# Kernel tuning notes

Hardware: AMD Instinct MI355X
Metric: run time of the kernel (lower is better)

The kernel has to match this reference:

```python
import jax, jax.numpy as jnp
import numpy as np

N, IN_DIM, ENC_DIM, K = 16384, 1024, 256, 8192


def setup_inputs() -> dict:
    key = jax.random.key(0)
    ks = jax.random.split(key, 10)
    s = 0.02
    return {
        "x": jax.random.normal(ks[0], (N, IN_DIM), dtype=jnp.float32),
        "enc_w1": jax.random.normal(ks[1], (IN_DIM, ENC_DIM), dtype=jnp.float32) * s,
        "enc_b1": jnp.zeros((ENC_DIM,), dtype=jnp.float32),
        "enc_w2": jax.random.normal(ks[2], (ENC_DIM, ENC_DIM), dtype=jnp.float32) * s,
        "enc_b2": jnp.zeros((ENC_DIM,), dtype=jnp.float32),
        "codewords": jax.random.normal(ks[3], (K, ENC_DIM), dtype=jnp.float32),
        "dec_w1": jax.random.normal(ks[4], (ENC_DIM, ENC_DIM), dtype=jnp.float32) * s,
        "dec_b1": jnp.zeros((ENC_DIM,), dtype=jnp.float32),
        "dec_w2": jax.random.normal(ks[5], (ENC_DIM, IN_DIM), dtype=jnp.float32) * s,
        "dec_b2": jnp.zeros((IN_DIM,), dtype=jnp.float32),
    }


def reference(x, enc_w1, enc_b1, enc_w2, enc_b2, codewords, dec_w1, dec_b1, dec_w2, dec_b2):
    # Encoder: Linear -> ReLU -> Linear -> ReLU
    h = jax.nn.relu(x @ enc_w1 + enc_b1)
    encoded = jax.nn.relu(h @ enc_w2 + enc_b2)  # [N, ENC_DIM]

    # VQ: full Euclidean distance matrix (torch.cdist, p=2), argmin, gather
    x2 = jnp.sum(encoded * encoded, axis=1, keepdims=True)          # [N, 1]
    c2 = jnp.sum(codewords * codewords, axis=1)                     # [K]
    d2 = x2 + c2[None, :] - 2.0 * (encoded @ codewords.T)           # [N, K]
    distances = jnp.sqrt(jnp.maximum(d2, 0.0))
    quantized_indices = jnp.argmin(distances, axis=1)               # [N] int
    quantized_distances = jnp.take_along_axis(
        distances, quantized_indices[:, None], axis=1)[:, 0]        # [N]
    quantized = codewords[quantized_indices]                        # [N, ENC_DIM]

    # Decoder: Linear -> ReLU -> Linear
    g = jax.nn.relu(quantized @ dec_w1 + dec_b1)
    reconstructed = g @ dec_w2 + dec_b2                              # [N, IN_DIM]
    return quantized_indices, quantized_distances, reconstructed, quantized
```

## Files before the change

### kernel.cpp

```cpp
#include <hip/hip_runtime.h>
#include <hip/hip_bf16.h>

#define NROWS   16384
#define IN_DIM  1024
#define ENC_DIM 256
#define KCW     8192
#define NCB     32

typedef __attribute__((ext_vector_type(8))) short short8v;
typedef __attribute__((ext_vector_type(4))) float f32x4;
typedef unsigned long long u64;
typedef unsigned int u32;

__device__ __forceinline__ unsigned short f2bf_rne(float x) {
    unsigned u = __float_as_uint(x);
    unsigned r = (u + 0x7fffu + ((u >> 16) & 1u)) >> 16;
    return (unsigned short)r;
}
__device__ __forceinline__ float bf2f(unsigned short h) {
    return __uint_as_float(((unsigned)h) << 16);
}
__device__ __forceinline__ int lex_lt(float d, int i, float D, int I) {
    return (d < D) || (d == D && i < I);
}
__device__ __forceinline__ void t2mrg(u64& b1, u64& b2, u64 c1, u64 c2) {
    u64 hi = (b1 > c1) ? b1 : c1;
    u64 lo2 = (b2 < c2) ? b2 : c2;
    b1 = (b1 < c1) ? b1 : c1;
    b2 = (hi < lo2) ? hi : lo2;
}
__device__ __forceinline__ void gload16(const void* g, void* l) {
    __builtin_amdgcn_global_load_lds(
        (__attribute__((address_space(1))) void*)g,
        (__attribute__((address_space(3))) void*)l, 16, 0, 0);
}

template<int K>
__device__ __forceinline__ void split_body(const float* __restrict__ src,
                                           unsigned short* __restrict__ dst,
                                           int e) {
    int row = e / (K / 4), kq = (e % (K / 4)) * 4;
    float4 v = ((const float4*)src)[e];
    ushort4 hi, lo;
    hi.x = f2bf_rne(v.x); lo.x = f2bf_rne(v.x - bf2f(hi.x));
    hi.y = f2bf_rne(v.y); lo.y = f2bf_rne(v.y - bf2f(hi.y));
    hi.z = f2bf_rne(v.z); lo.z = f2bf_rne(v.z - bf2f(hi.z));
    hi.w = f2bf_rne(v.w); lo.w = f2bf_rne(v.w - bf2f(hi.w));
    const int m = (row & 7) << 4;
    char* rowp = (char*)(dst + (size_t)row * (2 * K));
    int bh = kq * 2, bl = (K + kq) * 2;
    *(ushort4*)(rowp + ((bh & ~127) | ((bh & 127) ^ m))) = hi;
    *(ushort4*)(rowp + ((bl & ~127) | ((bl & 127) ^ m))) = lo;
}

template<int K>
__device__ __forceinline__ void tsplit_body(const float* __restrict__ W,
                                            unsigned short* __restrict__ Wt,
                                            int Ncols, int idx) {
    int n = idx / (K / 4), k4 = (idx % (K / 4)) * 4;
    float vx = W[(size_t)(k4 + 0) * Ncols + n];
    float vy = W[(size_t)(k4 + 1) * Ncols + n];
    float vz = W[(size_t)(k4 + 2) * Ncols + n];
    float vw = W[(size_t)(k4 + 3) * Ncols + n];
    ushort4 hi, lo;
    hi.x = f2bf_rne(vx); lo.x = f2bf_rne(vx - bf2f(hi.x));
    hi.y = f2bf_rne(vy); lo.y = f2bf_rne(vy - bf2f(hi.y));
    hi.z = f2bf_rne(vz); lo.z = f2bf_rne(vz - bf2f(hi.z));
    hi.w = f2bf_rne(vw); lo.w = f2bf_rne(vw - bf2f(hi.w));
    const int m = (n & 7) << 4;
    char* rp = (char*)(Wt + (size_t)n * (2 * K));
    int bh = k4 * 2, bl = (K + k4) * 2;
    *(ushort4*)(rp + ((bh & ~127) | ((bh & 127) ^ m))) = hi;
    *(ushort4*)(rp + ((bl & ~127) | ((bl & 127) ^ m))) = lo;
}

__device__ __forceinline__ void rownorm_body(const float* __restrict__ A,
                                             float* __restrict__ out, int idx) {
    int wid = idx >> 6, lane = idx & 63;
    float4 v = *(const float4*)(A + (size_t)wid * 256 + lane * 4);
    float s = (v.x * v.x + v.y * v.y) + (v.z * v.z + v.w * v.w);
#pragma unroll
    for (int off = 1; off < 64; off <<= 1) s += __shfl_xor(s, off);
    if (lane == 0) out[wid] = s;
}

__global__ __launch_bounds__(256)
void prep_all(const float* __restrict__ ew1, const float* __restrict__ ew2,
              const float* __restrict__ dw1, const float* __restrict__ dw2,
              const float* __restrict__ cw,
              unsigned short* __restrict__ w1ts, unsigned short* __restrict__ ew2t,
              unsigned short* __restrict__ dw1t, unsigned short* __restrict__ dw2t,
              unsigned short* __restrict__ Be,   float* __restrict__ c2) {
    int idx = blockIdx.x * 256 + threadIdx.x;
    if (idx < 65536)        { tsplit_body<1024>(ew1, w1ts, 256, idx); }
    else if (idx < 81920)   { tsplit_body<256>(ew2, ew2t, 256, idx - 65536); }
    else if (idx < 98304)   { tsplit_body<256>(dw1, dw1t, 256, idx - 81920); }
    else if (idx < 163840)  { tsplit_body<256>(dw2, dw2t, 1024, idx - 98304); }
    else if (idx < 688128)  { split_body<256>(cw, Be, idx - 163840); }
    else if (idx < 1212416) { rownorm_body(cw, c2, idx - 688128); }
}

struct MMP {
    const unsigned short* A;
    const unsigned short* Bt;
    const float* bias;
    float* C;
    unsigned short* Cs;
    int N, ars, brs, crs, KQ, EPI, gx;
};

__device__ void mm_device512(const MMP p, int bx, int by, int tid) {
    __shared__ __align__(16) unsigned short As[128][64];
    __shared__ __align__(16) unsigned short Bs[128][64];
    const int lane = tid & 63;
    const int wid = tid >> 6;
    const int wr = wid >> 2, wc = wid & 3;
    const int brow = by * 128;
    const int bcol = bx * 128;
    const int K = p.KQ * 64;

    f32x4 acc[4][2] = {};

    const int fr = tid >> 3;
    const int fk = (tid & 7) * 8;
    const int swz = (lane & 7) << 4;
    const int arow = wr * 64 + (lane & 15);
    const int brw  = wc * 32 + (lane & 15);
    const int klane = (lane >> 4) * 16;

    bool first = true;
#pragma unroll
    for (int term = 0; term < 3; ++term) {
        const int kaT = (term == 2) ? K : 0;
        const int kbT = (term == 1) ? K : 0;
        for (int kq = 0; kq < p.KQ; ++kq) {
            if (!first) __syncthreads();
            first = false;
            const int ka0 = kaT + kq * 64;
            const int kb0 = kbT + kq * 64;
#pragma unroll
            for (int l = 0; l < 2; ++l) {
                gload16(p.A  + (size_t)(brow + l * 64 + fr) * p.ars + ka0 + fk,
                        (char*)&As[0][0] + l * 8192 + tid * 16);
                gload16(p.Bt + (size_t)(bcol + l * 64 + fr) * p.brs + kb0 + fk,
                        (char*)&Bs[0][0] + l * 8192 + tid * 16);
            }
            __syncthreads();
#pragma unroll
            for (int kk = 0; kk < 2; ++kk) {
                const int kb = (kk * 64 + klane) ^ swz;
                short8v af[4], bfv[2];
#pragma unroll
                for (int mi = 0; mi < 4; mi++)
                    af[mi] = *(const short8v*)((const char*)&As[arow + mi * 16][0] + kb);
#pragma unroll
                for (int ni = 0; ni < 2; ni++)
                    bfv[ni] = *(const short8v*)((const char*)&Bs[brw + ni * 16][0] + kb);
#pragma unroll
                for (int mi = 0; mi < 4; mi++)
#pragma unroll
                    for (int ni = 0; ni < 2; ni++)
                        acc[mi][ni] = __builtin_amdgcn_mfma_f32_16x16x32_bf16(
                            af[mi], bfv[ni], acc[mi][ni], 0, 0, 0);
            }
        }
    }

#pragma unroll
    for (int mi = 0; mi < 4; mi++) {
#pragma unroll
        for (int q = 0; q < 4; q++) {
            int row = brow + wr * 64 + mi * 16 + (lane >> 4) * 4 + q;
            const int m = (row & 7) << 4;
            char* rp = (char*)(p.Cs + (size_t)row * p.crs);
#pragma unroll
            for (int ni = 0; ni < 2; ni++) {
                int col = bcol + wc * 32 + ni * 16 + (lane & 15);
                float v = acc[mi][ni][q] + p.bias[col];
                if (p.EPI != 3) v = fmaxf(v, 0.f);
                if (p.EPI & 1) p.C[(size_t)row * p.N + col] = v;
                if (p.EPI != 3) {
                    unsigned short hi = f2bf_rne(v);
                    int bh = col * 2;
                    *(unsigned short*)(rp + ((bh & ~127) | ((bh & 127) ^ m))) = hi;
                    if (p.EPI == 2) {
                        unsigned short lo = f2bf_rne(v - bf2f(hi));
                        int bl = (256 + col) * 2;
                        *(unsigned short*)(rp + ((bl & ~127) | ((bl & 127) ^ m))) = lo;
                    }
                }
            }
        }
    }
}

__global__ __launch_bounds__(512)
void mm_pair(MMP p0, MMP p1, int n0) {
    if ((int)blockIdx.x < n0) {
        mm_device512(p0, blockIdx.x % p0.gx, blockIdx.x / p0.gx, threadIdx.x);
    } else {
        int b = blockIdx.x - n0;
        mm_device512(p1, b % p1.gx, b / p1.gx, threadIdx.x);
    }
}

__global__ __launch_bounds__(512)
void enc1_fused(const float* __restrict__ x,
                const unsigned short* __restrict__ w1ts,
                const float* __restrict__ bias,
                unsigned short* __restrict__ Hs) {
    __shared__ __align__(16) unsigned short Ah[64][64];
    __shared__ __align__(16) unsigned short Al[64][64];
    __shared__ __align__(16) unsigned short Bh[256][64];
    __shared__ __align__(16) unsigned short Bl[256][64];
    const int tid = threadIdx.x;
    const int lane = tid & 63;
    const int wid = tid >> 6;
    const int wr = wid >> 2, wc = wid & 3;
    const int brow = blockIdx.x * 64;

    f32x4 acc[2][4] = {};

    const int fr = tid >> 3;
    const int fk = (tid & 7) * 8;
    const int swz = (lane & 7) << 4;
    const int arow = wr * 32 + (lane & 15);
    const int brw  = wc * 64 + (lane & 15);
    const int klane = (lane >> 4) * 16;
    const int aoff = fr * 128 + ((fk * 2) ^ ((fr & 7) << 4));

    float4 c0, c1, n0, n1;
    {
        const float* xp = x + (size_t)(brow + fr) * 1024 + fk;
        c0 = *(const float4*)xp; c1 = *(const float4*)(xp + 4);
    }

    for (int s = 0; s < 16; ++s) {
        const int k0 = s * 64;
        if (s) __syncthreads();
        {
            float vv[8] = { c0.x, c0.y, c0.z, c0.w, c1.x, c1.y, c1.z, c1.w };
            short8v uh, ul;
#pragma unroll
            for (int i = 0; i < 8; i++) {
                unsigned short h = f2bf_rne(vv[i]);
                uh[i] = (short)h;
                ul[i] = (short)f2bf_rne(vv[i] - bf2f(h));
            }
            *(short8v*)((char*)&Ah[0][0] + aoff) = uh;
            *(short8v*)((char*)&Al[0][0] + aoff) = ul;
        }
#pragma unroll
        for (int l = 0; l < 4; ++l) {
            gload16(w1ts + (size_t)(l * 64 + fr) * 2048 + k0 + fk,
                    (char*)&Bh[0][0] + l * 8192 + tid * 16);
            gload16(w1ts + (size_t)(l * 64 + fr) * 2048 + 1024 + k0 + fk,
                    (char*)&Bl[0][0] + l * 8192 + tid * 16);
        }
        if (s + 1 < 16) {
            const float* xp = x + (size_t)(brow + fr) * 1024 + k0 + 64 + fk;
            n0 = *(const float4*)xp; n1 = *(const float4*)(xp + 4);
        }
        __syncthreads();
#pragma unroll
        for (int kk = 0; kk < 2; ++kk) {
            const int kb = (kk * 64 + klane) ^ swz;
            short8v ah[2], al[2], bh[4], bl[4];
#pragma unroll
            for (int mi = 0; mi < 2; mi++) {
                ah[mi] = *(const short8v*)((const char*)&Ah[arow + mi * 16][0] + kb);
                al[mi] = *(const short8v*)((const char*)&Al[arow + mi * 16][0] + kb);
            }
#pragma unroll
            for (int ni = 0; ni < 4; ni++) {
                bh[ni] = *(const short8v*)((const char*)&Bh[brw + ni * 16][0] + kb);
                bl[ni] = *(const short8v*)((const char*)&Bl[brw + ni * 16][0] + kb);
            }
#pragma unroll
            for (int mi = 0; mi < 2; mi++)
#pragma unroll
                for (int ni = 0; ni < 4; ni++) {
                    acc[mi][ni] = __builtin_amdgcn_mfma_f32_16x16x32_bf16(
                        ah[mi], bh[ni], acc[mi][ni], 0, 0, 0);
                    acc[mi][ni] = __builtin_amdgcn_mfma_f32_16x16x32_bf16(
                        ah[mi], bl[ni], acc[mi][ni], 0, 0, 0);
                    acc[mi][ni] = __builtin_amdgcn_mfma_f32_16x16x32_bf16(
                        al[mi], bh[ni], acc[mi][ni], 0, 0, 0);
                }
        }
        c0 = n0; c1 = n1;
    }

#pragma unroll
    for (int mi = 0; mi < 2; mi++) {
#pragma unroll
        for (int q = 0; q < 4; q++) {
            int row = brow + wr * 32 + mi * 16 + (lane >> 4) * 4 + q;
            const int m = (row & 7) << 4;
            char* rp = (char*)(Hs + (size_t)row * 512);
#pragma unroll
            for (int ni = 0; ni < 4; ni++) {
                int col = wc * 64 + ni * 16 + (lane & 15);
                float v = fmaxf(acc[mi][ni][q] + bias[col], 0.f);
                unsigned short hi = f2bf_rne(v);
                unsigned short lo = f2bf_rne(v - bf2f(hi));
                int bh_ = col * 2, bl_ = (256 + col) * 2;
                *(unsigned short*)(rp + ((bh_ & ~127) | ((bh_ & 127) ^ m))) = hi;
                *(unsigned short*)(rp + ((bl_ & ~127) | ((bl_ & 127) ^ m))) = lo;
            }
        }
    }
}

__global__ __launch_bounds__(512)
void vq_mfma(const unsigned short* __restrict__ Ae,
             const unsigned short* __restrict__ Be,
             const float* __restrict__ c2,
             ulonglong2* __restrict__ part) {
    __shared__ __align__(16) unsigned short As[128][64];
    __shared__ __align__(16) unsigned short Bs[256][64];
    __shared__ u32 s1[128][4];
    __shared__ u32 s2[128][4];

    const int tid  = threadIdx.x;
    const int lane = tid & 63;
    const int wid  = tid >> 6;
    const int wr   = wid >> 2;
    const int wc   = wid & 3;
    const int brow = blockIdx.y * 128;
    const int bcol = blockIdx.x * 256;

    f32x4 acc[4][4] = {};

    const int fr = tid >> 3;
    const int fk = (tid & 7) * 8;
    const int swz   = (lane & 7) << 4;
    const int arow  = wr * 64 + (lane & 15);
    const int brw   = wc * 64 + (lane & 15);
    const int klane = (lane >> 4) * 16;

    for (int s = 0; s < 4; ++s) {
        const int k0 = s * 64;
        if (s) __syncthreads();
#pragma unroll
        for (int l = 0; l < 2; ++l)
            gload16(Ae + (size_t)(brow + l * 64 + fr) * 256 + k0 + fk,
                    (char*)&As[0][0] + l * 8192 + tid * 16);
#pragma unroll
        for (int l = 0; l < 4; ++l)
            gload16(Be + (size_t)(bcol + l * 64 + fr) * 512 + k0 + fk,
                    (char*)&Bs[0][0] + l * 8192 + tid * 16);
        __syncthreads();
#pragma unroll
        for (int kk = 0; kk < 2; ++kk) {
            const int kb = (kk * 64 + klane) ^ swz;
            short8v af[4], bfv[4];
#pragma unroll
            for (int mi = 0; mi < 4; mi++)
                af[mi] = *(const short8v*)((const char*)&As[arow + mi * 16][0] + kb);
#pragma unroll
            for (int ni = 0; ni < 4; ni++)
                bfv[ni] = *(const short8v*)((const char*)&Bs[brw + ni * 16][0] + kb);
#pragma unroll
            for (int mi = 0; mi < 4; mi++)
#pragma unroll
                for (int ni = 0; ni < 4; ni++)
                    acc[mi][ni] = __builtin_amdgcn_mfma_f32_16x16x32_bf16(
                        bfv[ni], af[mi], acc[mi][ni], 0, 0, 0);
        }
    }

    const int qrow = lane & 15;
    const int cq   = (lane >> 4) * 4;
    float4 c2q[4];
#pragma unroll
    for (int ni = 0; ni < 4; ni++)
        c2q[ni] = *(const float4*)&c2[bcol + wc * 64 + ni * 16 + cq];

#pragma unroll
    for (int mi = 0; mi < 4; mi++) {
        u32 b1 = 0xFFFFFFFFu, b2 = 0xFFFFFFFFu;
#pragma unroll
        for (int ni = 0; ni < 4; ni++) {
            const float* cp = (const float*)&c2q[ni];
#pragma unroll
            for (int r = 0; r < 4; r++) {
                float dk = fmaf(-2.0f, acc[mi][ni][r], cp[r]);
                dk = fmaxf(dk, 0.0f);
                u32 k = (__float_as_uint(dk) & ~255u)
                      | (u32)(wc * 64 + ni * 16 + cq + r);
                u32 mx = max(k, b1);
                b1 = min(k, b1);
                b2 = min(mx, b2);
            }
        }
#pragma unroll
        for (int off = 16; off < 64; off <<= 1) {
            u32 o1 = __shfl_xor(b1, off);
            u32 o2 = __shfl_xor(b2, off);
            u32 mx = max(b1, o1);
            b1 = min(b1, o1);
            b2 = min(min(b2, o2), mx);
        }
        if (lane < 16) {
            int rl = wr * 64 + mi * 16 + qrow;
            s1[rl][wc] = b1;
            s2[rl][wc] = b2;
        }
    }
    __syncthreads();
    if (tid < 128) {
        u32 b1 = s1[tid][0], b2 = s2[tid][0];
#pragma unroll
        for (int w = 1; w < 4; w++) {
            u32 c1 = s1[tid][w], cc2 = s2[tid][w];
            u32 mx = max(b1, c1);
            b1 = min(b1, c1);
            b2 = min(min(b2, cc2), mx);
        }
        ulonglong2 pk;
        pk.x = ((u64)b1 << 32) | (u32)(bcol + (b1 & 255u));
        pk.y = ((u64)b2 << 32) | (u32)(bcol + (b2 & 255u));
        part[(size_t)(brow + tid) * NCB + blockIdx.x] = pk;
    }
}

__global__ __launch_bounds__(512)
void combine_dec2(const ulonglong2* __restrict__ part,
                  const float* __restrict__ enc,
                  const float* __restrict__ cw,
                  const float* __restrict__ c2,
                  float* __restrict__ outIdx,
                  float* __restrict__ outDist,
                  int* __restrict__ idx32,
                  float* __restrict__ outQ,
                  MMP pd, int nd2) {
    if ((int)blockIdx.x < nd2) {
        mm_device512(pd, blockIdx.x % pd.gx, blockIdx.x / pd.gx, threadIdx.x);
        return;
    }
    const int row  = (blockIdx.x - nd2) * 8 + (threadIdx.x >> 6);
    const int lane = threadIdx.x & 63;

    u64 b1 = ~0ull, b2 = ~0ull;
    if (lane < NCB) {
        ulonglong2 pk = part[(size_t)row * NCB + lane];
        b1 = pk.x; b2 = pk.y;
    }
#pragma unroll
    for (int off = 1; off < 64; off <<= 1) {
        u64 c1 = __shfl_xor(b1, off);
        u64 cc2 = __shfl_xor(b2, off);
        t2mrg(b1, b2, c1, cc2);
    }
    int j1 = (int)(b1 & 0xffffffffu);
    int j2 = (int)(b2 & 0xffffffffu);

    float4 e4 = ((const float4*)(enc + (size_t)row * 256))[lane];
    float4 w1 = ((const float4*)(cw + (size_t)j1 * 256))[lane];
    float4 w2 = ((const float4*)(cw + (size_t)j2 * 256))[lane];
    float s1 = fmaf(e4.x, w1.x, fmaf(e4.y, w1.y, fmaf(e4.z, w1.z, e4.w * w1.w)));
    float s2 = fmaf(e4.x, w2.x, fmaf(e4.y, w2.y, fmaf(e4.z, w2.z, e4.w * w2.w)));
    float sx = (e4.x * e4.x + e4.y * e4.y) + (e4.z * e4.z + e4.w * e4.w);
#pragma unroll
    for (int off = 1; off < 64; off <<= 1) {
        s1 += __shfl_xor(s1, off);
        s2 += __shfl_xor(s2, off);
        sx += __shfl_xor(sx, off);
    }
    float d1 = sqrtf(fmaxf(sx + c2[j1] - 2.0f * s1, 0.f));
    float d2 = sqrtf(fmaxf(sx + c2[j2] - 2.0f * s2, 0.f));
    float bd; int bi;
    if (lex_lt(d1, j1, d2, j2)) { bd = d1; bi = j1; }
    else                        { bd = d2; bi = j2; }
    float4 wq = (bi == j1) ? w1 : w2;
    ((float4*)(outQ + (size_t)row * ENC_DIM))[lane] = wq;
    if (lane == 0) {
        outIdx[row]  = (float)bi;
        outDist[row] = bd;
        idx32[row]   = bi;
    }
}

__global__ void gather_rec(const int* __restrict__ idx32,
                           const float* __restrict__ rec_all,
                           float* __restrict__ outRec) {
    int row = blockIdx.x * 4 + (threadIdx.x >> 6);
    int lane = threadIdx.x & 63;
    int j = idx32[row];
    const float4* src = (const float4*)(rec_all + (size_t)j * IN_DIM);
    float4* dst = (float4*)(outRec + (size_t)row * IN_DIM);
#pragma unroll
    for (int i = 0; i < 4; i++) dst[lane + 64 * i] = src[lane + 64 * i];
}

extern "C" void kernel_launch(void* const* d_in, const int* in_sizes, int n_in,
                              void* d_out, int out_size, void* d_ws, size_t ws_size,
                              hipStream_t stream) {
    const float* x   = (const float*)d_in[0];
    const float* ew1 = (const float*)d_in[1];
    const float* eb1 = (const float*)d_in[2];
    const float* ew2 = (const float*)d_in[3];
    const float* eb2 = (const float*)d_in[4];
    const float* cw  = (const float*)d_in[5];
    const float* dw1 = (const float*)d_in[6];
    const float* db1 = (const float*)d_in[7];
    const float* dw2 = (const float*)d_in[8];
    const float* db2 = (const float*)d_in[9];
    float* out = (float*)d_out;
    float* ws  = (float*)d_ws;

    float* outIdx  = out;
    float* outDist = out + NROWS;
    float* outRec  = out + 2 * NROWS;
    float* outQ    = out + 2 * NROWS + (size_t)NROWS * IN_DIM;

    float*          enc     = ws;
    unsigned short* Ae      = (unsigned short*)(ws + 4194304);
    unsigned short* Gs      = (unsigned short*)(ws + 6291456);
    unsigned short* Hs      = (unsigned short*)(ws + 8388608);
    ulonglong2*     part    = (ulonglong2*)(ws + 8388608);
    float*          rec_all = ws + 10485760;
    unsigned short* Be      = (unsigned short*)(ws + 18874368);
    unsigned short* w1ts    = (unsigned short*)(ws + 20971520);
    unsigned short* ew2t    = (unsigned short*)(ws + 21233664);
    unsigned short* dw1t    = (unsigned short*)(ws + 21299200);
    unsigned short* dw2t    = (unsigned short*)(ws + 21364736);
    float*          c2      = ws + 21626880;
    int*            idx32   = (int*)(ws + 21635072);

    MMP p_enc2 = { Hs, ew2t, eb2, enc, Ae, 256, 512, 512, 256, 4, 1, 2 };
    MMP p_dec1 = { Be, dw1t, db1, nullptr, Gs, 256, 512, 512, 512, 4, 2, 2 };
    MMP p_dec2 = { Gs, dw2t, db2, rec_all, nullptr, 1024, 512, 512, 0, 4, 3, 8 };

    prep_all<<<4736, 256, 0, stream>>>(ew1, ew2, dw1, dw2, cw,
                                       w1ts, ew2t, dw1t, dw2t, Be, c2);
    enc1_fused<<<256, 512, 0, stream>>>(x, w1ts, eb1, Hs);
    mm_pair<<<384, 512, 0, stream>>>(p_enc2, p_dec1, 256);
    vq_mfma<<<dim3(NCB, 128), 512, 0, stream>>>(Ae, Be, c2, part);
    combine_dec2<<<512 + 2048, 512, 0, stream>>>(part, enc, cw, c2,
                                                 outIdx, outDist, idx32, outQ,
                                                 p_dec2, 512);
    gather_rec<<<NROWS / 4, 256, 0, stream>>>(idx32, rec_all, outRec);
}
```

Measured before the change: 194.6 us.

## Triple-buffer VQ kernel loads and move dec1 GEMM into VQ launch

```diff
diff --git a/kernel.cpp b/kernel.cpp
--- a/kernel.cpp
+++ b/kernel.cpp
@@ -33,24 +33,6 @@
     __builtin_amdgcn_global_load_lds(
         (__attribute__((address_space(1))) void*)g,
         (__attribute__((address_space(3))) void*)l, 16, 0, 0);
-}
-
-template<int K>
-__device__ __forceinline__ void split_body(const float* __restrict__ src,
-                                           unsigned short* __restrict__ dst,
-                                           int e) {
-    int row = e / (K / 4), kq = (e % (K / 4)) * 4;
-    float4 v = ((const float4*)src)[e];
-    ushort4 hi, lo;
-    hi.x = f2bf_rne(v.x); lo.x = f2bf_rne(v.x - bf2f(hi.x));
-    hi.y = f2bf_rne(v.y); lo.y = f2bf_rne(v.y - bf2f(hi.y));
-    hi.z = f2bf_rne(v.z); lo.z = f2bf_rne(v.z - bf2f(hi.z));
-    hi.w = f2bf_rne(v.w); lo.w = f2bf_rne(v.w - bf2f(hi.w));
-    const int m = (row & 7) << 4;
-    char* rowp = (char*)(dst + (size_t)row * (2 * K));
-    int bh = kq * 2, bl = (K + kq) * 2;
-    *(ushort4*)(rowp + ((bh & ~127) | ((bh & 127) ^ m))) = hi;
-    *(ushort4*)(rowp + ((bl & ~127) | ((bl & 127) ^ m))) = lo;
 }
 
 template<int K>
@@ -74,16 +56,6 @@
     *(ushort4*)(rp + ((bl & ~127) | ((bl & 127) ^ m))) = lo;
 }
 
-__device__ __forceinline__ void rownorm_body(const float* __restrict__ A,
-                                             float* __restrict__ out, int idx) {
-    int wid = idx >> 6, lane = idx & 63;
-    float4 v = *(const float4*)(A + (size_t)wid * 256 + lane * 4);
-    float s = (v.x * v.x + v.y * v.y) + (v.z * v.z + v.w * v.w);
-#pragma unroll
-    for (int off = 1; off < 64; off <<= 1) s += __shfl_xor(s, off);
-    if (lane == 0) out[wid] = s;
-}
-
 __global__ __launch_bounds__(256)
 void prep_all(const float* __restrict__ ew1, const float* __restrict__ ew2,
               const float* __restrict__ dw1, const float* __restrict__ dw2,
@@ -96,8 +68,25 @@
     else if (idx < 81920)   { tsplit_body<256>(ew2, ew2t, 256, idx - 65536); }
     else if (idx < 98304)   { tsplit_body<256>(dw1, dw1t, 256, idx - 81920); }
     else if (idx < 163840)  { tsplit_body<256>(dw2, dw2t, 1024, idx - 98304); }
-    else if (idx < 688128)  { split_body<256>(cw, Be, idx - 163840); }
-    else if (idx < 1212416) { rownorm_body(cw, c2, idx - 688128); }
+    else if (idx < 688128) {
+        int e = idx - 163840;
+        int row = e >> 6, kq = (e & 63) * 4;
+        float4 v = ((const float4*)cw)[e];
+        ushort4 hi, lo;
+        hi.x = f2bf_rne(v.x); lo.x = f2bf_rne(v.x - bf2f(hi.x));
+        hi.y = f2bf_rne(v.y); lo.y = f2bf_rne(v.y - bf2f(hi.y));
+        hi.z = f2bf_rne(v.z); lo.z = f2bf_rne(v.z - bf2f(hi.z));
+        hi.w = f2bf_rne(v.w); lo.w = f2bf_rne(v.w - bf2f(hi.w));
+        const int m = (row & 7) << 4;
+        char* rowp = (char*)(Be + (size_t)row * 512);
+        int bh = kq * 2, bl = (256 + kq) * 2;
+        *(ushort4*)(rowp + ((bh & ~127) | ((bh & 127) ^ m))) = hi;
+        *(ushort4*)(rowp + ((bl & ~127) | ((bl & 127) ^ m))) = lo;
+        float s = (v.x * v.x + v.y * v.y) + (v.z * v.z + v.w * v.w);
+#pragma unroll
+        for (int off = 1; off < 64; off <<= 1) s += __shfl_xor(s, off);
+        if ((threadIdx.x & 63) == 0) c2[row] = s;
+    }
 }
 
 struct MMP {
@@ -109,9 +98,9 @@
     int N, ars, brs, crs, KQ, EPI, gx;
 };
 
-__device__ void mm_device512(const MMP p, int bx, int by, int tid) {
-    __shared__ __align__(16) unsigned short As[128][64];
-    __shared__ __align__(16) unsigned short Bs[128][64];
+__device__ void mm_device512(const MMP p, int bx, int by, int tid, char* lds) {
+    unsigned short (*As)[64] = (unsigned short(*)[64])lds;
+    unsigned short (*Bs)[64] = (unsigned short(*)[64])(lds + 16384);
     const int lane = tid & 63;
     const int wid = tid >> 6;
     const int wr = wid >> 2, wc = wid & 3;
@@ -195,13 +184,9 @@
 }
 
 __global__ __launch_bounds__(512)
-void mm_pair(MMP p0, MMP p1, int n0) {
-    if ((int)blockIdx.x < n0) {
-        mm_device512(p0, blockIdx.x % p0.gx, blockIdx.x / p0.gx, threadIdx.x);
-    } else {
-        int b = blockIdx.x - n0;
-        mm_device512(p1, b % p1.gx, b / p1.gx, threadIdx.x);
-    }
+void mm_one(MMP p) {
+    __shared__ __align__(16) char pool[32768];
+    mm_device512(p, blockIdx.x % p.gx, blockIdx.x / p.gx, threadIdx.x, pool);
 }
 
 __global__ __launch_bounds__(512)
@@ -316,21 +301,25 @@
 void vq_mfma(const unsigned short* __restrict__ Ae,
              const unsigned short* __restrict__ Be,
              const float* __restrict__ c2,
-             ulonglong2* __restrict__ part) {
-    __shared__ __align__(16) unsigned short As[128][64];
-    __shared__ __align__(16) unsigned short Bs[256][64];
-    __shared__ u32 s1[128][4];
-    __shared__ u32 s2[128][4];
-
+             ulonglong2* __restrict__ part,
+             MMP pd, int nvq) {
+    __shared__ __align__(16) char pool[151552];
+    if ((int)blockIdx.x >= nvq) {
+        int b = blockIdx.x - nvq;
+        mm_device512(pd, b % pd.gx, b / pd.gx, threadIdx.x, pool);
+        return;
+    }
     const int tid  = threadIdx.x;
     const int lane = tid & 63;
     const int wid  = tid >> 6;
     const int wr   = wid >> 2;
     const int wc   = wid & 3;
-    const int brow = blockIdx.y * 128;
-    const int bcol = blockIdx.x * 256;
-
-    f32x4 acc[4][4] = {};
+    const int bid  = blockIdx.x;
+    const int brow = (bid >> 5) * 128;
+    const int bcol = (bid & 31) * 256;
+
+    u32* s1 = (u32*)(pool + 147456);
+    u32* s2 = (u32*)(pool + 149504);
 
     const int fr = tid >> 3;
     const int fk = (tid & 7) * 8;
@@ -339,34 +328,58 @@
     const int brw   = wc * 64 + (lane & 15);
     const int klane = (lane >> 4) * 16;
 
-    for (int s = 0; s < 4; ++s) {
+    auto stage = [&](int s, int buf) {
+        char* A = pool + buf * 49152;
+        char* B = A + 16384;
         const int k0 = s * 64;
-        if (s) __syncthreads();
 #pragma unroll
         for (int l = 0; l < 2; ++l)
             gload16(Ae + (size_t)(brow + l * 64 + fr) * 256 + k0 + fk,
-                    (char*)&As[0][0] + l * 8192 + tid * 16);
+                    A + l * 8192 + tid * 16);
 #pragma unroll
         for (int l = 0; l < 4; ++l)
             gload16(Be + (size_t)(bcol + l * 64 + fr) * 512 + k0 + fk,
-                    (char*)&Bs[0][0] + l * 8192 + tid * 16);
-        __syncthreads();
+                    B + l * 8192 + tid * 16);
+    };
+
+    f32x4 acc[4][4] = {};
+
+    stage(0, 0);
+    stage(1, 1);
+    asm volatile("s_waitcnt vmcnt(6)" ::: "memory");
+    __builtin_amdgcn_s_barrier();
+
+#pragma unroll
+    for (int s = 0; s < 4; ++s) {
+        const int buf = s % 3;
+        if (s + 2 < 4) stage(s + 2, (s + 2) % 3);
+        const char* A = pool + buf * 49152;
+        const char* B = A + 16384;
+        __builtin_amdgcn_s_setprio(1);
 #pragma unroll
         for (int kk = 0; kk < 2; ++kk) {
             const int kb = (kk * 64 + klane) ^ swz;
             short8v af[4], bfv[4];
 #pragma unroll
             for (int mi = 0; mi < 4; mi++)
-                af[mi] = *(const short8v*)((const char*)&As[arow + mi * 16][0] + kb);
+                af[mi] = *(const short8v*)(A + (arow + mi * 16) * 128 + kb);
 #pragma unroll
             for (int ni = 0; ni < 4; ni++)
-                bfv[ni] = *(const short8v*)((const char*)&Bs[brw + ni * 16][0] + kb);
+                bfv[ni] = *(const short8v*)(B + (brw + ni * 16) * 128 + kb);
 #pragma unroll
             for (int mi = 0; mi < 4; mi++)
 #pragma unroll
                 for (int ni = 0; ni < 4; ni++)
                     acc[mi][ni] = __builtin_amdgcn_mfma_f32_16x16x32_bf16(
                         bfv[ni], af[mi], acc[mi][ni], 0, 0, 0);
+        }
+        __builtin_amdgcn_s_setprio(0);
+        if (s == 0 || s == 1) {
+            asm volatile("s_waitcnt vmcnt(6)" ::: "memory");
+            __builtin_amdgcn_s_barrier();
+        } else if (s == 2) {
+            asm volatile("s_waitcnt vmcnt(0)" ::: "memory");
+            __builtin_amdgcn_s_barrier();
         }
     }
 
@@ -404,16 +417,16 @@
         }
         if (lane < 16) {
             int rl = wr * 64 + mi * 16 + qrow;
-            s1[rl][wc] = b1;
-            s2[rl][wc] = b2;
+            s1[rl * 4 + wc] = b1;
+            s2[rl * 4 + wc] = b2;
         }
     }
     __syncthreads();
     if (tid < 128) {
-        u32 b1 = s1[tid][0], b2 = s2[tid][0];
+        u32 b1 = s1[tid * 4 + 0], b2 = s2[tid * 4 + 0];
 #pragma unroll
         for (int w = 1; w < 4; w++) {
-            u32 c1 = s1[tid][w], cc2 = s2[tid][w];
+            u32 c1 = s1[tid * 4 + w], cc2 = s2[tid * 4 + w];
             u32 mx = max(b1, c1);
             b1 = min(b1, c1);
             b2 = min(min(b2, cc2), mx);
@@ -421,7 +434,7 @@
         ulonglong2 pk;
         pk.x = ((u64)b1 << 32) | (u32)(bcol + (b1 & 255u));
         pk.y = ((u64)b2 << 32) | (u32)(bcol + (b2 & 255u));
-        part[(size_t)(brow + tid) * NCB + blockIdx.x] = pk;
+        part[(size_t)(brow + tid) * NCB + (bid & 31)] = pk;
     }
 }
 
@@ -435,8 +448,9 @@
                   int* __restrict__ idx32,
                   float* __restrict__ outQ,
                   MMP pd, int nd2) {
+    __shared__ __align__(16) char pool[32768];
     if ((int)blockIdx.x < nd2) {
-        mm_device512(pd, blockIdx.x % pd.gx, blockIdx.x / pd.gx, threadIdx.x);
+        mm_device512(pd, blockIdx.x % pd.gx, blockIdx.x / pd.gx, threadIdx.x, pool);
         return;
     }
     const int row  = (blockIdx.x - nd2) * 8 + (threadIdx.x >> 6);
@@ -533,11 +547,11 @@
     MMP p_dec1 = { Be, dw1t, db1, nullptr, Gs, 256, 512, 512, 512, 4, 2, 2 };
     MMP p_dec2 = { Gs, dw2t, db2, rec_all, nullptr, 1024, 512, 512, 0, 4, 3, 8 };
 
-    prep_all<<<4736, 256, 0, stream>>>(ew1, ew2, dw1, dw2, cw,
+    prep_all<<<2688, 256, 0, stream>>>(ew1, ew2, dw1, dw2, cw,
                                        w1ts, ew2t, dw1t, dw2t, Be, c2);
     enc1_fused<<<256, 512, 0, stream>>>(x, w1ts, eb1, Hs);
-    mm_pair<<<384, 512, 0, stream>>>(p_enc2, p_dec1, 256);
-    vq_mfma<<<dim3(NCB, 128), 512, 0, stream>>>(Ae, Be, c2, part);
+    mm_one<<<256, 512, 0, stream>>>(p_enc2);
+    vq_mfma<<<4096 + 128, 512, 0, stream>>>(Ae, Be, c2, part, p_dec1, 4096);
     combine_dec2<<<512 + 2048, 512, 0, stream>>>(part, enc, cw, c2,
                                                  outIdx, outDist, idx32, outQ,
                                                  p_dec2, 512);
```

Result: slower. 226.8 us (+16.6%).
